# Kernel optimization log

Measured on AMD Instinct MI355X. Metric: run time of the kernel, lower is better.

## Reference

```python
import jax, jax.numpy as jnp
import numpy as np

NUM_NODES = 20000
SEQ_LEN = 128
IN_FEATS = 2
HIDDEN = 32
N_TOTAL = NUM_NODES * SEQ_LEN  # flattened graph size
N_EDGES = 2_000_000


def setup_inputs() -> dict:
    key = jax.random.key(0)
    ks = jax.random.split(key, 10)
    x = jax.random.normal(ks[0], (NUM_NODES, SEQ_LEN, IN_FEATS), dtype=jnp.float32)
    edge_index = jax.random.randint(ks[1], (2, N_EDGES), 0, N_TOTAL, dtype=jnp.int64)
    s = 0.1
    gcn_W = jax.random.normal(ks[2], (IN_FEATS, HIDDEN), dtype=jnp.float32) * s
    gcn_b = jnp.zeros((HIDDEN,), dtype=jnp.float32)
    w_ih = jax.random.normal(ks[3], (4 * HIDDEN, HIDDEN), dtype=jnp.float32) * s
    w_hh = jax.random.normal(ks[4], (4 * HIDDEN, HIDDEN), dtype=jnp.float32) * s
    b_ih = jax.random.normal(ks[5], (4 * HIDDEN,), dtype=jnp.float32) * s
    b_hh = jax.random.normal(ks[6], (4 * HIDDEN,), dtype=jnp.float32) * s
    fc_W = jax.random.normal(ks[7], (HIDDEN, 1), dtype=jnp.float32) * s
    fc_b = jnp.zeros((1,), dtype=jnp.float32)
    return {"x": x, "edge_index": edge_index, "gcn_W": gcn_W, "gcn_b": gcn_b,
            "w_ih": w_ih, "w_hh": w_hh, "b_ih": b_ih, "b_hh": b_hh,
            "fc_W": fc_W, "fc_b": fc_b}


def _gcn(x_flat, edge_index, W, b):
    # PyG GCNConv: add self-loops, symmetric normalization, then linear+bias.
    src, dst = edge_index[0], edge_index[1]
    n = x_flat.shape[0]
    # degree at target side, including the self-loop (+1)
    deg = jax.ops.segment_sum(jnp.ones_like(dst, dtype=x_flat.dtype), dst, num_segments=n) + 1.0
    dinv = jax.lax.rsqrt(deg)  # deg >= 1 always (self-loop)
    h = x_flat @ W  # [n, HIDDEN] transform before propagate
    norm = dinv[src] * dinv[dst]  # [E]
    msg = h[src] * norm[:, None]  # gather + per-edge scale
    agg = jax.ops.segment_sum(msg, dst, num_segments=n)
    # self-loop contribution: dinv_i * dinv_i * h_i = h_i / deg_i
    out = agg + h * (1.0 / deg)[:, None]
    return out + b


def _lstm(xs, w_ih, w_hh, b_ih, b_hh):
    # torch LSTM gate order: i, f, g, o. xs: [N, S, H] -> final hidden [N, H]
    n, s, hdim = xs.shape
    xs_t = jnp.swapaxes(xs, 0, 1)  # [S, N, H]
    # precompute input projections once (dense GEMM)
    x_proj = xs_t @ w_ih.T + b_ih + b_hh  # [S, N, 4H]

    def step(carry, xp):
        h, c = carry
        g = xp + h @ w_hh.T  # [N, 4H]
        i, f, gg, o = jnp.split(g, 4, axis=-1)
        c = jax.nn.sigmoid(f) * c + jax.nn.sigmoid(i) * jnp.tanh(gg)
        h = jax.nn.sigmoid(o) * jnp.tanh(c)
        return (h, c), None

    h0 = jnp.zeros((n, hdim), dtype=xs.dtype)
    (hn, _), _ = jax.lax.scan(step, (h0, h0), x_proj)
    return hn


def reference(x, edge_index, gcn_W, gcn_b, w_ih, w_hh, b_ih, b_hh, fc_W, fc_b):
    num_nodes, seq_len, num_feats = x.shape
    x_in = x.reshape(-1, num_feats)  # [N*S, F]
    x_gcn = jax.nn.relu(_gcn(x_in, edge_index, gcn_W, gcn_b))
    x_lstm = x_gcn.reshape(num_nodes, seq_len, -1)
    hn = _lstm(x_lstm, w_ih, w_hh, b_ih, b_hh)
    return hn @ fc_W + fc_b  # [num_nodes, 1]
```

## Files before the change

### kernel.cpp

```cpp
#include <hip/hip_runtime.h>

#define SEQ 128
#define HID 32
#define TPB 256
#define XS 56

typedef __attribute__((ext_vector_type(8))) short short8;
typedef __attribute__((ext_vector_type(4))) float floatx4;


__global__ void count_kernel(const int* __restrict__ idx, int E, int* __restrict__ cnt) {
    int e = (blockIdx.x * blockDim.x + threadIdx.x) * 4;
    if (((E & 3) == 0) && e + 3 < E) {
        int4 d = *(const int4*)(idx + E + e);
        atomicAdd(&cnt[d.x], 1);
        atomicAdd(&cnt[d.y], 1);
        atomicAdd(&cnt[d.z], 1);
        atomicAdd(&cnt[d.w], 1);
    } else {
        int lim = min(e + 4, E);
        for (int k = e; k < lim; ++k) atomicAdd(&cnt[idx[E + k]], 1);
    }
}

__device__ __forceinline__ unsigned long long pk2(float xx, float yy, float dv) {
    int qx = __float2int_rn(xx * dv * 2097152.0f);
    int qy = __float2int_rn(yy * dv * 2097152.0f);
    return ((unsigned long long)(unsigned)(qx + (1 << 26)) << 32) |
           (unsigned)(qy + (1 << 26));
}

__global__ void scatter_pk_kernel(const int* __restrict__ idx, int E,
                                  const float2* __restrict__ x2,
                                  const int* __restrict__ deg,
                                  unsigned long long* __restrict__ aggP) {
    int e = (blockIdx.x * blockDim.x + threadIdx.x) * 4;
    if (((E & 3) == 0) && e + 3 < E) {
        int4 s = *(const int4*)(idx + e);
        int4 d = *(const int4*)(idx + E + e);
        float2 v0 = x2[s.x];
        float2 v1 = x2[s.y];
        float2 v2 = x2[s.z];
        float2 v3 = x2[s.w];
        float dv0 = rsqrtf((float)deg[s.x] + 1.0f);
        float dv1 = rsqrtf((float)deg[s.y] + 1.0f);
        float dv2 = rsqrtf((float)deg[s.z] + 1.0f);
        float dv3 = rsqrtf((float)deg[s.w] + 1.0f);
        atomicAdd(&aggP[d.x], pk2(v0.x, v0.y, dv0));
        atomicAdd(&aggP[d.y], pk2(v1.x, v1.y, dv1));
        atomicAdd(&aggP[d.z], pk2(v2.x, v2.y, dv2));
        atomicAdd(&aggP[d.w], pk2(v3.x, v3.y, dv3));
    } else {
        int lim = min(e + 4, E);
        for (int k = e; k < lim; ++k) {
            int s = idx[k];
            int d = idx[E + k];
            float2 v = x2[s];
            float dv = rsqrtf((float)deg[s] + 1.0f);
            atomicAdd(&aggP[d], pk2(v.x, v.y, dv));
        }
    }
}


__device__ __forceinline__ float sigm_f(float x) {
    return __builtin_amdgcn_rcpf(1.0f + __expf(-x));
}
__device__ __forceinline__ float tanh_f(float x) {
    return fmaf(__builtin_amdgcn_rcpf(1.0f + __expf(-2.0f * x)), 2.0f, -1.0f);
}
__device__ __forceinline__ void fsplit(float f, short& hi, short& lo) {
    unsigned u = __float_as_uint(f);
    hi = (short)(u >> 16);
    float r = f - __uint_as_float(u & 0xFFFF0000u);
    lo = (short)(__float_as_uint(r) >> 16);
}
__device__ __forceinline__ int pks(short a, short b) {
    return (int)(((unsigned)(unsigned short)b << 16) | (unsigned short)a);
}

__global__ __launch_bounds__(TPB, 4) void lstm_gs_kernel(
    const float2* __restrict__ x2,
    const unsigned long long* __restrict__ aggP, const int* __restrict__ deg,
    int N,
    const float* __restrict__ gcn_W, const float* __restrict__ gcn_b,
    const float* __restrict__ w_ih, const float* __restrict__ w_hh,
    const float* __restrict__ b_ih, const float* __restrict__ b_hh,
    const float* __restrict__ fc_W, const float* __restrict__ fc_b,
    float* __restrict__ out) {
    __shared__ float2 ubuf[16][SEQ + 1];
    __shared__ float pre[4][32][17];
    __shared__ __align__(16) short hhb[16][XS];
    __shared__ __align__(16) short hlb[16][XS];
    __shared__ __align__(16) short xgb[16][XS];
    __shared__ __align__(16) short xlb[16][XS];
    __shared__ float fcp[4][16];

    const int tid = threadIdx.x;
    const int w = tid >> 6;
    const int lane = tid & 63;
    const int n = lane & 15;
    const int q = lane >> 4;
    const int base = blockIdx.x * 16;

    {
        const float2* xb = x2 + (size_t)base * SEQ;
        const unsigned long long* apb = aggP + (size_t)base * SEQ;
        const int* dgb = deg + (size_t)base * SEQ;
        const int lim = min(16 * SEQ, (N - base) * SEQ);
        for (int i = tid; i < 16 * SEQ; i += TPB) {
            float2 v = make_float2(0.f, 0.f);
            if (i < lim) {
                int dg = dgb[i];
                float dv = rsqrtf((float)dg + 1.0f);
                float2 xx = xb[i];
                unsigned long long pk = apb[i];
                unsigned bias = (unsigned)dg * 67108864u;
                float ax = (float)((int)((unsigned)(pk >> 32) - bias)) * (1.0f / 2097152.0f);
                float ay = (float)((int)((unsigned)pk - bias)) * (1.0f / 2097152.0f);
                v = make_float2(dv * fmaf(xx.x, dv, ax), dv * fmaf(xx.y, dv, ay));
            }
            ubuf[i >> 7][i & 127] = v;
        }
        if (tid < 16) ubuf[tid][SEQ] = make_float2(0.f, 0.f);
    }

    short8 AiH[2], AiL[2], AhH[2], AhL[2];
    floatx4 biasC[2];
    #pragma unroll
    for (int t1 = 0; t1 < 2; ++t1) {
        const int arow = w * 32 + 16 * t1 + n;
        const float* wi = w_ih + arow * HID + 8 * q;
        const float* wh = w_hh + arow * HID + 8 * q;
        #pragma unroll
        for (int j = 0; j < 8; ++j) {
            short h16, l16;
            fsplit(wi[j], h16, l16); AiH[t1][j] = h16; AiL[t1][j] = l16;
            fsplit(wh[j], h16, l16); AhH[t1][j] = h16; AhL[t1][j] = l16;
        }
        #pragma unroll
        for (int r = 0; r < 4; ++r) {
            const int brow = w * 32 + 16 * t1 + 4 * q + r;
            biasC[t1][r] = b_ih[brow] + b_hh[brow];
        }
    }

    const int ua = 8 * w + 2 * q;
    const float wg0a = gcn_W[ua],       wg0b = gcn_W[ua + 1];
    const float wg1a = gcn_W[HID + ua], wg1b = gcn_W[HID + ua + 1];
    const float gbca = gcn_b[ua],       gbcb = gcn_b[ua + 1];
    const float fcwa = fc_W[ua],        fcwb = fc_W[ua + 1];

    float c0 = 0.f, c1 = 0.f, ho0 = 0.f, ho1 = 0.f;

    __syncthreads();

    *(int*)&hhb[n][ua] = 0;
    *(int*)&hlb[n][ua] = 0;
    {
        float2 uu = ubuf[n][0];
        float ga = fmaxf(fmaf(uu.x, wg0a, fmaf(uu.y, wg1a, gbca)), 0.f);
        float gb = fmaxf(fmaf(uu.x, wg0b, fmaf(uu.y, wg1b, gbcb)), 0.f);
        short gah, gal, gbh, gbl;
        fsplit(ga, gah, gal); fsplit(gb, gbh, gbl);
        *(int*)&xgb[n][ua] = pks(gah, gbh);
        *(int*)&xlb[n][ua] = pks(gal, gbl);
    }
    __syncthreads();

    floatx4 aX[2];
    {
        const short8 xh = *(const short8*)&xgb[n][8 * q];
        const short8 xl = *(const short8*)&xlb[n][8 * q];
        __builtin_amdgcn_s_setprio(1);
        #pragma unroll
        for (int t1 = 0; t1 < 2; ++t1)
            aX[t1] = __builtin_amdgcn_mfma_f32_16x16x32_bf16(AiH[t1], xh, biasC[t1], 0, 0, 0);
        #pragma unroll
        for (int t1 = 0; t1 < 2; ++t1)
            aX[t1] = __builtin_amdgcn_mfma_f32_16x16x32_bf16(AiL[t1], xh, aX[t1], 0, 0, 0);
        #pragma unroll
        for (int t1 = 0; t1 < 2; ++t1)
            aX[t1] = __builtin_amdgcn_mfma_f32_16x16x32_bf16(AiH[t1], xl, aX[t1], 0, 0, 0);
        __builtin_amdgcn_s_setprio(0);
    }

    #pragma unroll 1
    for (int t = 0; t < SEQ; ++t) {
        {
            const short8 hh = *(const short8*)&hhb[n][8 * q];
            const short8 hl = *(const short8*)&hlb[n][8 * q];
            floatx4 acc[2];
            __builtin_amdgcn_s_setprio(1);
            #pragma unroll
            for (int t1 = 0; t1 < 2; ++t1)
                acc[t1] = __builtin_amdgcn_mfma_f32_16x16x32_bf16(AhH[t1], hh, aX[t1], 0, 0, 0);
            #pragma unroll
            for (int t1 = 0; t1 < 2; ++t1)
                acc[t1] = __builtin_amdgcn_mfma_f32_16x16x32_bf16(AhL[t1], hh, acc[t1], 0, 0, 0);
            #pragma unroll
            for (int t1 = 0; t1 < 2; ++t1)
                acc[t1] = __builtin_amdgcn_mfma_f32_16x16x32_bf16(AhH[t1], hl, acc[t1], 0, 0, 0);
            __builtin_amdgcn_s_setprio(0);
            float av[8];
            #pragma unroll
            for (int t1 = 0; t1 < 2; ++t1)
                #pragma unroll
                for (int r = 0; r < 4; ++r) av[4 * t1 + r] = acc[t1][r];
            if (w == 2) {
                #pragma unroll
                for (int k = 0; k < 8; ++k) av[k] = tanh_f(av[k]);
            } else {
                #pragma unroll
                for (int k = 0; k < 8; ++k) av[k] = sigm_f(av[k]);
            }
            #pragma unroll
            for (int t1 = 0; t1 < 2; ++t1)
                #pragma unroll
                for (int r = 0; r < 4; ++r)
                    pre[w][16 * t1 + 4 * q + r][n] = av[4 * t1 + r];
        }
        __syncthreads();

        {
            const float i0 = pre[0][ua][n],     f0 = pre[1][ua][n];
            const float g0 = pre[2][ua][n],     o0 = pre[3][ua][n];
            const float i1 = pre[0][ua + 1][n], f1 = pre[1][ua + 1][n];
            const float g1 = pre[2][ua + 1][n], o1 = pre[3][ua + 1][n];
            c0 = fmaf(f0, c0, i0 * g0);
            c1 = fmaf(f1, c1, i1 * g1);
            const float h0 = o0 * tanh_f(c0);
            const float h1 = o1 * tanh_f(c1);
            ho0 = h0; ho1 = h1;
            short h0h, h0l, h1h, h1l;
            fsplit(h0, h0h, h0l); fsplit(h1, h1h, h1l);
            *(int*)&hhb[n][ua] = pks(h0h, h1h);
            *(int*)&hlb[n][ua] = pks(h0l, h1l);
            float2 uu = ubuf[n][t + 1];
            float ga = fmaxf(fmaf(uu.x, wg0a, fmaf(uu.y, wg1a, gbca)), 0.f);
            float gb = fmaxf(fmaf(uu.x, wg0b, fmaf(uu.y, wg1b, gbcb)), 0.f);
            short gah, gal, gbh, gbl;
            fsplit(ga, gah, gal); fsplit(gb, gbh, gbl);
            *(int*)&xgb[n][ua] = pks(gah, gbh);
            *(int*)&xlb[n][ua] = pks(gal, gbl);
        }
        __syncthreads();

        {
            const short8 xh = *(const short8*)&xgb[n][8 * q];
            const short8 xl = *(const short8*)&xlb[n][8 * q];
            __builtin_amdgcn_s_setprio(1);
            #pragma unroll
            for (int t1 = 0; t1 < 2; ++t1)
                aX[t1] = __builtin_amdgcn_mfma_f32_16x16x32_bf16(AiH[t1], xh, biasC[t1], 0, 0, 0);
            #pragma unroll
            for (int t1 = 0; t1 < 2; ++t1)
                aX[t1] = __builtin_amdgcn_mfma_f32_16x16x32_bf16(AiL[t1], xh, aX[t1], 0, 0, 0);
            #pragma unroll
            for (int t1 = 0; t1 < 2; ++t1)
                aX[t1] = __builtin_amdgcn_mfma_f32_16x16x32_bf16(AiH[t1], xl, aX[t1], 0, 0, 0);
            __builtin_amdgcn_s_setprio(0);
        }
    }

    float partial = fmaf(ho0, fcwa, ho1 * fcwb);
    partial += __shfl_xor(partial, 16);
    partial += __shfl_xor(partial, 32);
    if (lane < 16) fcp[w][lane] = partial;
    __syncthreads();
    if (w == 0 && lane < 16) {
        const int node = base + lane;
        if (node < N)
            out[node] = fcp[0][lane] + fcp[1][lane] + fcp[2][lane] + fcp[3][lane] + fc_b[0];
    }
}

extern "C" void kernel_launch(void* const* d_in, const int* in_sizes, int n_in,
                              void* d_out, int out_size, void* d_ws, size_t ws_size,
                              hipStream_t stream) {
    const float* x     = (const float*)d_in[0];
    const int*   idx   = (const int*)d_in[1];
    const float* gcn_W = (const float*)d_in[2];
    const float* gcn_b = (const float*)d_in[3];
    const float* w_ih  = (const float*)d_in[4];
    const float* w_hh  = (const float*)d_in[5];
    const float* b_ih  = (const float*)d_in[6];
    const float* b_hh  = (const float*)d_in[7];
    const float* fc_W  = (const float*)d_in[8];
    const float* fc_b  = (const float*)d_in[9];

    const int num_nodes = in_sizes[0] / (SEQ * 2);
    const int ntot = num_nodes * SEQ;
    const int E = in_sizes[1] / 2;

    int* deg = (int*)d_ws;
    unsigned long long* aggP = (unsigned long long*)((char*)d_ws + (size_t)ntot * 4);

    hipMemsetAsync(d_ws, 0, (size_t)ntot * 12, stream);

    const int eb = (E + 1023) / 1024;
    count_kernel<<<eb, 256, 0, stream>>>(idx, E, deg);
    scatter_pk_kernel<<<eb, 256, 0, stream>>>(idx, E, (const float2*)x, deg, aggP);
    lstm_gs_kernel<<<(num_nodes + 15) / 16, TPB, 0, stream>>>(
        (const float2*)x, aggP, deg, num_nodes,
        gcn_W, gcn_b, w_ih, w_hh, b_ih, b_hh, fc_W, fc_b,
        (float*)d_out);
}
```

Baseline: 484.3 us.

## Stream per-step GCN inputs from global with register prefetch instead of LDS staging

Drops the 16x129 float2 shared-memory staging buffer and the up-front load/normalize loop. Each thread now loads aggP, deg and x for its node directly from global memory one timestep ahead, keeping them in registers and computing the GCN normalization inline. It also raises launch_bounds occupancy from 4 to 5 blocks per CU and pads the pre buffer stride from 17 to 20. The intent is to cut LDS footprint and the prologue latency and to overlap the loads with the recurrence. The cost is per-step scattered global loads, with each node's row read redundantly by the four wave lanes that share it, plus extra registers.

Measured after the change: 515.0 us. 6.4% more time.

```diff
diff --git a/kernel.cpp b/kernel.cpp
--- a/kernel.cpp
+++ b/kernel.cpp
@@ -4,6 +4,7 @@
 #define HID 32
 #define TPB 256
 #define XS 56
+#define PS 20
 
 typedef __attribute__((ext_vector_type(8))) short short8;
 typedef __attribute__((ext_vector_type(4))) float floatx4;
@@ -79,7 +80,7 @@
     return (int)(((unsigned)(unsigned short)b << 16) | (unsigned short)a);
 }
 
-__global__ __launch_bounds__(TPB, 4) void lstm_gs_kernel(
+__global__ __launch_bounds__(TPB, 5) void lstm_gs2_kernel(
     const float2* __restrict__ x2,
     const unsigned long long* __restrict__ aggP, const int* __restrict__ deg,
     int N,
@@ -88,8 +89,7 @@
     const float* __restrict__ b_ih, const float* __restrict__ b_hh,
     const float* __restrict__ fc_W, const float* __restrict__ fc_b,
     float* __restrict__ out) {
-    __shared__ float2 ubuf[16][SEQ + 1];
-    __shared__ float pre[4][32][17];
+    __shared__ float pre[4][32][PS];
     __shared__ __align__(16) short hhb[16][XS];
     __shared__ __align__(16) short hlb[16][XS];
     __shared__ __align__(16) short xgb[16][XS];
@@ -103,27 +103,10 @@
     const int q = lane >> 4;
     const int base = blockIdx.x * 16;
 
-    {
-        const float2* xb = x2 + (size_t)base * SEQ;
-        const unsigned long long* apb = aggP + (size_t)base * SEQ;
-        const int* dgb = deg + (size_t)base * SEQ;
-        const int lim = min(16 * SEQ, (N - base) * SEQ);
-        for (int i = tid; i < 16 * SEQ; i += TPB) {
-            float2 v = make_float2(0.f, 0.f);
-            if (i < lim) {
-                int dg = dgb[i];
-                float dv = rsqrtf((float)dg + 1.0f);
-                float2 xx = xb[i];
-                unsigned long long pk = apb[i];
-                unsigned bias = (unsigned)dg * 67108864u;
-                float ax = (float)((int)((unsigned)(pk >> 32) - bias)) * (1.0f / 2097152.0f);
-                float ay = (float)((int)((unsigned)pk - bias)) * (1.0f / 2097152.0f);
-                v = make_float2(dv * fmaf(xx.x, dv, ax), dv * fmaf(xx.y, dv, ay));
-            }
-            ubuf[i >> 7][i & 127] = v;
-        }
-        if (tid < 16) ubuf[tid][SEQ] = make_float2(0.f, 0.f);
-    }
+    const int nd = min(base + n, N - 1);
+    const unsigned long long* apb = aggP + (size_t)nd * SEQ;
+    const int* dgb = deg + (size_t)nd * SEQ;
+    const float2* xpb = x2 + (size_t)nd * SEQ;
 
     short8 AiH[2], AiL[2], AhH[2], AhL[2];
     floatx4 biasC[2];
@@ -153,19 +136,30 @@
 
     float c0 = 0.f, c1 = 0.f, ho0 = 0.f, ho1 = 0.f;
 
-    __syncthreads();
-
-    *(int*)&hhb[n][ua] = 0;
-    *(int*)&hlb[n][ua] = 0;
     {
-        float2 uu = ubuf[n][0];
-        float ga = fmaxf(fmaf(uu.x, wg0a, fmaf(uu.y, wg1a, gbca)), 0.f);
-        float gb = fmaxf(fmaf(uu.x, wg0b, fmaf(uu.y, wg1b, gbcb)), 0.f);
+        int d0 = dgb[0];
+        unsigned long long a0 = apb[0];
+        float2 xx0 = xpb[0];
+        float dv = rsqrtf((float)d0 + 1.0f);
+        unsigned bias = (unsigned)d0 * 67108864u;
+        float ax = (float)((int)((unsigned)(a0 >> 32) - bias)) * (1.0f / 2097152.0f);
+        float ay = (float)((int)((unsigned)a0 - bias)) * (1.0f / 2097152.0f);
+        float ux = dv * fmaf(xx0.x, dv, ax);
+        float uy = dv * fmaf(xx0.y, dv, ay);
+        float ga = fmaxf(fmaf(ux, wg0a, fmaf(uy, wg1a, gbca)), 0.f);
+        float gb = fmaxf(fmaf(ux, wg0b, fmaf(uy, wg1b, gbcb)), 0.f);
         short gah, gal, gbh, gbl;
         fsplit(ga, gah, gal); fsplit(gb, gbh, gbl);
         *(int*)&xgb[n][ua] = pks(gah, gbh);
         *(int*)&xlb[n][ua] = pks(gal, gbl);
     }
+    *(int*)&hhb[n][ua] = 0;
+    *(int*)&hlb[n][ua] = 0;
+
+    unsigned long long pa = apb[1];
+    int pd = dgb[1];
+    float2 px = xpb[1];
+
     __syncthreads();
 
     floatx4 aX[2];
@@ -236,13 +230,22 @@
             fsplit(h0, h0h, h0l); fsplit(h1, h1h, h1l);
             *(int*)&hhb[n][ua] = pks(h0h, h1h);
             *(int*)&hlb[n][ua] = pks(h0l, h1l);
-            float2 uu = ubuf[n][t + 1];
-            float ga = fmaxf(fmaf(uu.x, wg0a, fmaf(uu.y, wg1a, gbca)), 0.f);
-            float gb = fmaxf(fmaf(uu.x, wg0b, fmaf(uu.y, wg1b, gbcb)), 0.f);
+            float dv = rsqrtf((float)pd + 1.0f);
+            unsigned bias = (unsigned)pd * 67108864u;
+            float ax = (float)((int)((unsigned)(pa >> 32) - bias)) * (1.0f / 2097152.0f);
+            float ay = (float)((int)((unsigned)pa - bias)) * (1.0f / 2097152.0f);
+            float ux = dv * fmaf(px.x, dv, ax);
+            float uy = dv * fmaf(px.y, dv, ay);
+            float ga = fmaxf(fmaf(ux, wg0a, fmaf(uy, wg1a, gbca)), 0.f);
+            float gb = fmaxf(fmaf(ux, wg0b, fmaf(uy, wg1b, gbcb)), 0.f);
             short gah, gal, gbh, gbl;
             fsplit(ga, gah, gal); fsplit(gb, gbh, gbl);
             *(int*)&xgb[n][ua] = pks(gah, gbh);
             *(int*)&xlb[n][ua] = pks(gal, gbl);
+            const int tt = min(t + 2, SEQ - 1);
+            pa = apb[tt];
+            pd = dgb[tt];
+            px = xpb[tt];
         }
         __syncthreads();
 
@@ -301,7 +304,7 @@
     const int eb = (E + 1023) / 1024;
     count_kernel<<<eb, 256, 0, stream>>>(idx, E, deg);
     scatter_pk_kernel<<<eb, 256, 0, stream>>>(idx, E, (const float2*)x, deg, aggP);
-    lstm_gs_kernel<<<(num_nodes + 15) / 16, TPB, 0, stream>>>(
+    lstm_gs2_kernel<<<(num_nodes + 15) / 16, TPB, 0, stream>>>(
         (const float2*)x, aggP, deg, num_nodes,
         gcn_W, gcn_b, w_ih, w_hh, b_ih, b_hh, fc_W, fc_b,
         (float*)d_out);
```
